# Performance work log

Measured on AMD Instinct MI355X. Metric: run time of the kernel, lower is better.

## Reference

```python
import jax, jax.numpy as jnp
import numpy as np

DIM = 512
HEADS = 8
HEAD_DIM = DIM // HEADS
WINDOW = 128
TOKEN_SELF_ATTN_VALUE = -5e4  # lucidrains local-attention constant for shared_qk self mask


def setup_inputs() -> dict:
    key = jax.random.key(0)
    k1, k2, k3, k4 = jax.random.split(key, 4)
    B, N = 4, 8192
    x = jax.random.normal(k1, (B, N, DIM), dtype=jnp.float32)
    w_qkv = jax.random.normal(k2, (3 * DIM, DIM), dtype=jnp.float32) * (DIM ** -0.5)
    w_proj = jax.random.normal(k3, (DIM, DIM), dtype=jnp.float32) * (DIM ** -0.5)
    b_proj = jax.random.normal(k4, (DIM,), dtype=jnp.float32) * 0.01
    return {"x": x, "w_qkv": w_qkv, "w_proj": w_proj, "b_proj": b_proj}


def _look_around(b):
    # b: [B,H,nw,w,D] -> [B,H,nw,2w,D] = concat(prev_window, cur_window); window 0 padded with zeros
    padded = jnp.pad(b, ((0, 0), (0, 0), (1, 0), (0, 0), (0, 0)))
    return jnp.concatenate([padded[:, :, :-1], b], axis=3)


def _local_attn(q, k, v):
    # causal sliding-window attention, window=128, look_backward=1, shared_qk
    B, H, N, D = q.shape
    w = WINDOW
    nw = N // w
    scale = D ** -0.5
    # shared_qk: l2-normalize keys (F.normalize, eps=1e-12)
    k = k / jnp.clip(jnp.linalg.norm(k, axis=-1, keepdims=True), 1e-12, None)

    bq = q.reshape(B, H, nw, w, D)
    bk = _look_around(k.reshape(B, H, nw, w, D))  # [B,H,nw,2w,D]
    bv = _look_around(v.reshape(B, H, nw, w, D))

    t = jnp.arange(N).reshape(nw, w)
    t_pad = jnp.pad(t, ((1, 0), (0, 0)), constant_values=-1)
    bq_t = t                                         # [nw, w]
    bq_k = jnp.concatenate([t_pad[:-1], t], axis=1)  # [nw, 2w]

    sim = jnp.einsum('bhwie,bhwje->bhwij', bq, bk) * scale  # [B,H,nw,w,2w]

    self_mask = bq_t[:, :, None] == bq_k[:, None, :]
    causal_mask = bq_t[:, :, None] < bq_k[:, None, :]
    pad_mask = (bq_k == -1)[:, None, :]
    mask_value = -jnp.finfo(sim.dtype).max
    sim = jnp.where(self_mask, TOKEN_SELF_ATTN_VALUE, sim)
    sim = jnp.where(causal_mask | pad_mask, mask_value, sim)

    attn = jax.nn.softmax(sim, axis=-1)  # dropout is identity in eval mode
    out = jnp.einsum('bhwij,bhwje->bhwie', attn, bv)
    return out.reshape(B, H, N, D)


def reference(x, w_qkv, w_proj, b_proj):
    B, N, C = x.shape
    qkv = x @ w_qkv.T  # [B,N,3C]
    q, k, v = jnp.split(qkv, 3, axis=-1)
    to_heads = lambda t: t.reshape(B, N, HEADS, HEAD_DIM).transpose(0, 2, 1, 3)
    out = _local_attn(to_heads(q), to_heads(k), to_heads(v))  # [B,H,N,D]
    out = out.transpose(0, 2, 1, 3).reshape(B, N, C)
    return out @ w_proj.T + b_proj
```

## Files before the change

### kernel.cpp

```cpp
#include <hip/hip_runtime.h>
#include <stdint.h>

typedef uint16_t u16;
typedef __bf16 bf16x8 __attribute__((ext_vector_type(8)));
typedef float f32x4 __attribute__((ext_vector_type(4)));
typedef uint16_t u16x4 __attribute__((ext_vector_type(4)));
typedef uint16_t u16x8 __attribute__((ext_vector_type(8)));

typedef __attribute__((address_space(1))) void as1_void;
typedef __attribute__((address_space(3))) void as3_void;

__device__ __forceinline__ float bf2f(u16 b) {
    union { uint32_t u; float f; } v; v.u = ((uint32_t)b) << 16; return v.f;
}
__device__ __forceinline__ u16 f2bf(float f) {
    union { float f; uint32_t u; } v; v.f = f;
    uint32_t u = v.u;
    u += 0x7fffu + ((u >> 16) & 1u);
    return (u16)(u >> 16);
}
__device__ __forceinline__ void gload_lds16(const u16* g, u16* l) {
    __builtin_amdgcn_global_load_lds((as1_void*)g, (as3_void*)l, 16, 0, 0);
}

__global__ __launch_bounds__(256) void cvt3(
    const float* __restrict__ x,  u16* __restrict__ xb,
    const float* __restrict__ wq, u16* __restrict__ wqb,
    const float* __restrict__ wp, u16* __restrict__ wpb)
{
    const float* src; u16* dst; int base, nb;
    const int b = blockIdx.x;
    if (b < 1024)      { src = x;  dst = xb;  base = b;        nb = 1024; }
    else if (b < 1072) { src = wq; dst = wqb; base = b - 1024; nb = 48;   }
    else               { src = wp; dst = wpb; base = b - 1072; nb = 16;   }
    size_t i = ((size_t)base * 256 + threadIdx.x) * 8;
    const size_t stride = (size_t)nb * 256 * 8;
    #pragma unroll
    for (int it = 0; it < 8; ++it, i += stride) {
        f32x4 a = *(const f32x4*)(src + i);
        f32x4 c = *(const f32x4*)(src + i + 4);
        u16x8 o;
        o[0] = f2bf(a[0]); o[1] = f2bf(a[1]); o[2] = f2bf(a[2]); o[3] = f2bf(a[3]);
        o[4] = f2bf(c[0]); o[5] = f2bf(c[1]); o[6] = f2bf(c[2]); o[7] = f2bf(c[3]);
        *(u16x8*)(dst + i) = o;
    }
}

template<int NT, bool C_F32, bool NORMK>
__global__ __launch_bounds__(256, 2) void gemm128(
    const u16* __restrict__ A, int lda,
    const u16* __restrict__ B, int ldb,
    const float* __restrict__ bias,
    void* __restrict__ Cv, int ldc)
{
    __shared__ u16 lA[2][128 * 64];
    __shared__ u16 lB[2][128 * 64];

    const int tid  = threadIdx.x;
    const int lane = tid & 63;
    const int wave = tid >> 6;
    const int wr = (wave >> 1) * 64;
    const int wc = (wave & 1) * 64;
    const int cl = lane & 15;
    const int gr = lane >> 4;

    int fid = blockIdx.y * gridDim.x + blockIdx.x;
    const int nwg = gridDim.x * gridDim.y;
    fid = (fid & 7) * (nwg >> 3) + (fid >> 3);
    const int row0 = (fid / gridDim.x) * 128;
    const int col0 = (fid % gridDim.x) * 128;

    const int srow   = lane >> 3;
    const int schunk = ((lane & 7) - srow) & 7;

    f32x4 acc[4][4] = {};

    auto STAGE = [&](int t, int d) {
        const int k0 = t * 64;
        #pragma unroll
        for (int i = 0; i < 4; ++i) {
            const int Rg = wave * 32 + i * 8;
            gload_lds16(A + (size_t)(row0 + Rg + srow) * lda + k0 + schunk * 8,
                        &lA[d][Rg * 64]);
            gload_lds16(B + (size_t)(col0 + Rg + srow) * ldb + k0 + schunk * 8,
                        &lB[d][Rg * 64]);
        }
    };

    auto COMPUTE = [&](int d) {
        const u16* la = lA[d];
        const u16* lb = lB[d];
        bf16x8 bfrag[2][4];
        #pragma unroll
        for (int kk = 0; kk < 2; ++kk)
            #pragma unroll
            for (int n = 0; n < 4; ++n) {
                const int rb = wc + n * 16 + cl;
                bfrag[kk][n] = *(const bf16x8*)(lb + rb * 64 + (((kk * 4 + gr + rb) & 7) * 8));
            }
        __builtin_amdgcn_s_setprio(1);
        #pragma unroll
        for (int m = 0; m < 4; ++m) {
            const int ra = wr + m * 16 + cl;
            const bf16x8 a0 = *(const bf16x8*)(la + ra * 64 + (((gr + ra) & 7) * 8));
            const bf16x8 a1 = *(const bf16x8*)(la + ra * 64 + (((4 + gr + ra) & 7) * 8));
            #pragma unroll
            for (int n = 0; n < 4; ++n)
                acc[m][n] = __builtin_amdgcn_mfma_f32_16x16x32_bf16(a0, bfrag[0][n], acc[m][n], 0, 0, 0);
            #pragma unroll
            for (int n = 0; n < 4; ++n)
                acc[m][n] = __builtin_amdgcn_mfma_f32_16x16x32_bf16(a1, bfrag[1][n], acc[m][n], 0, 0, 0);
        }
        __builtin_amdgcn_s_setprio(0);
    };

    STAGE(0, 0);
    STAGE(1, 1);
    #pragma unroll
    for (int t = 0; t < NT; ++t) {
        if (t < NT - 1) asm volatile("s_waitcnt vmcnt(8)" ::: "memory");
        else            asm volatile("s_waitcnt vmcnt(0)" ::: "memory");
        __builtin_amdgcn_s_barrier();
        COMPUTE(t & 1);
        __builtin_amdgcn_s_barrier();
        if (t + 2 < NT) STAGE(t + 2, t & 1);
    }

    if constexpr (NORMK) {
        if (col0 + wc >= 512 && col0 + wc < 1024) {
            #pragma unroll
            for (int m = 0; m < 4; ++m)
                #pragma unroll
                for (int j = 0; j < 4; ++j) {
                    float ss = 0.f;
                    #pragma unroll
                    for (int n = 0; n < 4; ++n) ss += acc[m][n][j] * acc[m][n][j];
                    ss += __shfl_xor(ss, 1);
                    ss += __shfl_xor(ss, 2);
                    ss += __shfl_xor(ss, 4);
                    ss += __shfl_xor(ss, 8);
                    const float scl = 1.f / fmaxf(sqrtf(ss), 1e-12f);
                    #pragma unroll
                    for (int n = 0; n < 4; ++n) acc[m][n][j] *= scl;
                }
        }
    }

    #pragma unroll
    for (int m = 0; m < 4; ++m) {
        const int r = row0 + wr + m * 16 + gr * 4;
        #pragma unroll
        for (int n = 0; n < 4; ++n) {
            const int c = col0 + wc + n * 16 + cl;
            const float bv = bias ? bias[c] : 0.f;
            #pragma unroll
            for (int j = 0; j < 4; ++j) {
                const float val = acc[m][n][j] + bv;
                if constexpr (C_F32) ((float*)Cv)[(size_t)(r + j) * ldc + c] = val;
                else                 ((u16*)Cv)[(size_t)(r + j) * ldc + c] = f2bf(val);
            }
        }
    }
}

template<bool A_F32, bool C_F32, bool NORMK>
__global__ __launch_bounds__(256) void gemm_bt_f32(
    const void* __restrict__ Av, int lda,
    const float* __restrict__ B, int ldb,
    const float* __restrict__ bias,
    void* __restrict__ Cv, int ldc,
    int K)
{
    __shared__ u16 lA[128 * 32];
    __shared__ u16 lB[128 * 32];

    const int tid  = threadIdx.x;
    const int lane = tid & 63;
    const int wave = tid >> 6;
    const int wr   = (wave >> 1) * 64;
    const int wc   = (wave & 1) * 64;
    const int row0 = blockIdx.y * 128;
    const int col0 = blockIdx.x * 128;

    f32x4 acc[4][4] = {};

    for (int k0 = 0; k0 < K; k0 += 32) {
        #pragma unroll
        for (int i = 0; i < 4; ++i) {
            const int idx = i * 256 + tid;
            const int r = idx >> 3;
            const int p = (idx & 7) * 4;
            u16x4 a4, b4;
            if constexpr (A_F32) {
                const float* Af = (const float*)Av;
                f32x4 va = *(const f32x4*)(Af + (size_t)(row0 + r) * lda + k0 + p);
                a4[0] = f2bf(va[0]); a4[1] = f2bf(va[1]); a4[2] = f2bf(va[2]); a4[3] = f2bf(va[3]);
            } else {
                const u16* Ab = (const u16*)Av;
                a4 = *(const u16x4*)(Ab + (size_t)(row0 + r) * lda + k0 + p);
            }
            {
                f32x4 vb = *(const f32x4*)(B + (size_t)(col0 + r) * ldb + k0 + p);
                b4[0] = f2bf(vb[0]); b4[1] = f2bf(vb[1]); b4[2] = f2bf(vb[2]); b4[3] = f2bf(vb[3]);
            }
            *(u16x4*)&lA[r * 32 + p] = a4;
            *(u16x4*)&lB[r * 32 + p] = b4;
        }
        __syncthreads();

        bf16x8 af[4], bfv[4];
        #pragma unroll
        for (int m = 0; m < 4; ++m)
            af[m] = *(const bf16x8*)(lA + (wr + m * 16 + (lane & 15)) * 32 + (lane >> 4) * 8);
        #pragma unroll
        for (int n = 0; n < 4; ++n)
            bfv[n] = *(const bf16x8*)(lB + (wc + n * 16 + (lane & 15)) * 32 + (lane >> 4) * 8);
        #pragma unroll
        for (int m = 0; m < 4; ++m)
            #pragma unroll
            for (int n = 0; n < 4; ++n)
                acc[m][n] = __builtin_amdgcn_mfma_f32_16x16x32_bf16(af[m], bfv[n], acc[m][n], 0, 0, 0);
        __syncthreads();
    }

    if constexpr (NORMK) {
        if (col0 >= 512 && col0 < 1024) {
            #pragma unroll
            for (int m = 0; m < 4; ++m)
                #pragma unroll
                for (int j = 0; j < 4; ++j) {
                    float ss = 0.f;
                    #pragma unroll
                    for (int n = 0; n < 4; ++n) ss += acc[m][n][j] * acc[m][n][j];
                    ss += __shfl_xor(ss, 1);
                    ss += __shfl_xor(ss, 2);
                    ss += __shfl_xor(ss, 4);
                    ss += __shfl_xor(ss, 8);
                    const float scl = 1.f / fmaxf(sqrtf(ss), 1e-12f);
                    #pragma unroll
                    for (int n = 0; n < 4; ++n) acc[m][n][j] *= scl;
                }
        }
    }

    #pragma unroll
    for (int m = 0; m < 4; ++m) {
        const int r = row0 + wr + m * 16 + ((lane >> 4) << 2);
        #pragma unroll
        for (int n = 0; n < 4; ++n) {
            const int c = col0 + wc + n * 16 + (lane & 15);
            const float bv = bias ? bias[c] : 0.f;
            #pragma unroll
            for (int j = 0; j < 4; ++j) {
                const float val = acc[m][n][j] + bv;
                if constexpr (C_F32) ((float*)Cv)[(size_t)(r + j) * ldc + c] = val;
                else                 ((u16*)Cv)[(size_t)(r + j) * ldc + c] = f2bf(val);
            }
        }
    }
}

__global__ __launch_bounds__(512, 4) void attn_kernel(const u16* qkv, u16* o)
{
    constexpr int CC = 1536;
    constexpr int NTOK = 8192;
    constexpr int KP = 72;
    constexpr int VP = 136;
    constexpr int PP = 136;
    __shared__ u16 kn[128 * KP];
    __shared__ u16 vT[64 * VP];
    __shared__ u16 Pl[128 * PP];

    const int tid  = threadIdx.x;
    const int lane = tid & 63;
    const int wave = tid >> 6;
    const int cl = lane & 15;
    const int gr = lane >> 4;

    int blk = blockIdx.x;
    blk = (blk & 7) * (gridDim.x >> 3) + (blk >> 3);

    const int iw  = blk & 63;
    const int h   = (blk >> 6) & 7;
    const int b   = blk >> 9;

    const int tq0 = iw * 128;
    const size_t rowbase = (size_t)b * NTOK;
    const u16* qbase = qkv + rowbase * CC + h * 64;
    const u16* kbase = qbase + 512;
    const u16* vbase = qbase + 1024;

    const int wrow = wave * 16;
    bf16x8 qf[2];
    #pragma unroll
    for (int kk = 0; kk < 2; ++kk)
        qf[kk] = *(const bf16x8*)(qbase + (size_t)(tq0 + wrow + cl) * CC + kk * 32 + gr * 8);

    f32x4 oacc[4] = {};
    float m_run[4] = {-3.0e38f, -3.0e38f, -3.0e38f, -3.0e38f};
    float l_run[4] = {0.f, 0.f, 0.f, 0.f};

    for (int c = 0; c < 2; ++c) {
        const int tkc = tq0 - 128 + c * 128;

        #pragma unroll
        for (int p = 0; p < 2; ++p) {
            const int id = tid + p * 512;
            const int row = id >> 3, dc = id & 7;
            u16x8 v8 = {};
            if (tkc >= 0) v8 = *(const u16x8*)(kbase + (size_t)(tkc + row) * CC + dc * 8);
            *(u16x8*)&kn[row * KP + dc * 8] = v8;
        }
        #pragma unroll
        for (int p = 0; p < 2; ++p) {
            const int id = tid + p * 512;
            const int key = id & 127, dc = id >> 7;
            u16x8 v8 = {};
            if (tkc >= 0) v8 = *(const u16x8*)(vbase + (size_t)(tkc + key) * CC + dc * 8);
            #pragma unroll
            for (int e = 0; e < 8; ++e) vT[(dc * 8 + e) * VP + key] = v8[e];
        }
        __syncthreads();

        f32x4 s[8] = {};
        #pragma unroll
        for (int n = 0; n < 8; ++n)
            #pragma unroll
            for (int kk = 0; kk < 2; ++kk) {
                const bf16x8 kf = *(const bf16x8*)&kn[(n * 16 + cl) * KP + kk * 32 + gr * 8];
                s[n] = __builtin_amdgcn_mfma_f32_16x16x32_bf16(qf[kk], kf, s[n], 0, 0, 0);
            }

        float pmax[4] = {-3.0e38f, -3.0e38f, -3.0e38f, -3.0e38f};
        #pragma unroll
        for (int n = 0; n < 8; ++n) {
            const int tkk = tkc + n * 16 + cl;
            const bool pad = tkk < 0;
            #pragma unroll
            for (int j = 0; j < 4; ++j) {
                const int tq = tq0 + wrow + gr * 4 + j;
                float sv = s[n][j] * 0.125f;
                const int rel = tkk - tq;
                sv = (rel == 0) ? -5.0e4f : sv;
                sv = (rel > 0 || pad) ? -6.0e4f : sv;
                s[n][j] = sv;
                pmax[j] = fmaxf(pmax[j], sv);
            }
        }
        float cold[4];
        #pragma unroll
        for (int j = 0; j < 4; ++j) {
            pmax[j] = fmaxf(pmax[j], __shfl_xor(pmax[j], 1));
            pmax[j] = fmaxf(pmax[j], __shfl_xor(pmax[j], 2));
            pmax[j] = fmaxf(pmax[j], __shfl_xor(pmax[j], 4));
            pmax[j] = fmaxf(pmax[j], __shfl_xor(pmax[j], 8));
            const float mn = fmaxf(m_run[j], pmax[j]);
            cold[j] = __expf(m_run[j] - mn);
            m_run[j] = mn;
            l_run[j] *= cold[j];
        }
        #pragma unroll
        for (int n = 0; n < 8; ++n)
            #pragma unroll
            for (int j = 0; j < 4; ++j) {
                const float p = __expf(s[n][j] - m_run[j]);
                s[n][j] = p;
                l_run[j] += p;
            }
        #pragma unroll
        for (int n = 0; n < 4; ++n) {
            f32x4 t = oacc[n];
            t[0] *= cold[0]; t[1] *= cold[1]; t[2] *= cold[2]; t[3] *= cold[3];
            oacc[n] = t;
        }
        #pragma unroll
        for (int n = 0; n < 8; ++n)
            #pragma unroll
            for (int j = 0; j < 4; ++j)
                Pl[(wrow + gr * 4 + j) * PP + n * 16 + cl] = f2bf(s[n][j]);
        __syncthreads();

        #pragma unroll
        for (int kk = 0; kk < 4; ++kk) {
            const bf16x8 pa = *(const bf16x8*)&Pl[(wrow + cl) * PP + kk * 32 + gr * 8];
            #pragma unroll
            for (int n = 0; n < 4; ++n) {
                const bf16x8 vb = *(const bf16x8*)&vT[(n * 16 + cl) * VP + kk * 32 + gr * 8];
                oacc[n] = __builtin_amdgcn_mfma_f32_16x16x32_bf16(pa, vb, oacc[n], 0, 0, 0);
            }
        }
        __syncthreads();
    }

    float inv[4];
    #pragma unroll
    for (int j = 0; j < 4; ++j) {
        l_run[j] += __shfl_xor(l_run[j], 1);
        l_run[j] += __shfl_xor(l_run[j], 2);
        l_run[j] += __shfl_xor(l_run[j], 4);
        l_run[j] += __shfl_xor(l_run[j], 8);
        inv[j] = 1.f / l_run[j];
    }
    u16* obase = o + rowbase * CC + h * 64;
    const int r0 = tq0 + wrow + gr * 4;
    #pragma unroll
    for (int n = 0; n < 4; ++n) {
        const int d = n * 16 + cl;
        #pragma unroll
        for (int j = 0; j < 4; ++j)
            obase[(size_t)(r0 + j) * CC + d] = f2bf(oacc[n][j] * inv[j]);
    }
}

extern "C" void kernel_launch(void* const* d_in, const int* in_sizes, int n_in,
                              void* d_out, int out_size, void* d_ws, size_t ws_size,
                              hipStream_t stream)
{
    (void)in_sizes; (void)n_in; (void)out_size;
    const float* x      = (const float*)d_in[0];
    const float* w_qkv  = (const float*)d_in[1];
    const float* w_proj = (const float*)d_in[2];
    const float* b_proj = (const float*)d_in[3];
    float* out = (float*)d_out;

    const int BN = 4 * 8192;
    const size_t qkv_b = (size_t)BN * 1536 * 2;
    const size_t xb_b  = (size_t)BN * 512 * 2;
    const size_t wq_b  = (size_t)1536 * 512 * 2;
    const size_t wp_b  = (size_t)512 * 512 * 2;

    uint8_t* p = (uint8_t*)d_ws;
    u16* qkv = (u16*)p;

    if (ws_size >= qkv_b + xb_b + wq_b + wp_b) {
        u16* xb  = (u16*)(p + qkv_b);
        u16* wqb = (u16*)(p + qkv_b + xb_b);
        u16* wpb = (u16*)(p + qkv_b + xb_b + wq_b);
        cvt3<<<1088, 256, 0, stream>>>(x, xb, w_qkv, wqb, w_proj, wpb);
        gemm128<8, false, true><<<dim3(12, 256), 256, 0, stream>>>(
            xb, 512, wqb, 512, nullptr, qkv, 1536);
        attn_kernel<<<dim3(4 * 8 * 64), 512, 0, stream>>>(qkv, qkv);
        gemm128<8, true, false><<<dim3(4, 256), 256, 0, stream>>>(
            qkv, 1536, wpb, 512, b_proj, out, 512);
    } else {
        gemm_bt_f32<true, false, true><<<dim3(12, BN / 128), 256, 0, stream>>>(
            x, 512, w_qkv, 512, nullptr, qkv, 1536, 512);
        attn_kernel<<<dim3(4 * 8 * 64), 512, 0, stream>>>(qkv, qkv);
        gemm_bt_f32<false, true, false><<<dim3(4, BN / 128), 256, 0, stream>>>(
            qkv, 1536, w_proj, 512, b_proj, out, 512, 512);
    }
}
```

Before: 190.0 us.

## Load GEMM B operand directly into registers instead of staging through LDS

The bf16 GEMM no longer stages the weight (B) tile in shared memory. Each wave now loads its B fragments straight from global memory into registers, software-prefetched one k-step ahead, while A is still double-buffered in LDS. This halves LDS usage and the LDS read traffic per block and removes the B cooperative loads. The cost is redundant global/L2 reads of B across the waves and blocks that share it, more registers held live, and hand-tuned vmcnt wait counts that must match the new number of outstanding loads.

```diff
diff --git a/kernel.cpp b/kernel.cpp
--- a/kernel.cpp
+++ b/kernel.cpp
@@ -47,14 +47,13 @@
 }
 
 template<int NT, bool C_F32, bool NORMK>
-__global__ __launch_bounds__(256, 2) void gemm128(
+__global__ __launch_bounds__(256, 2) void gemm_breg(
     const u16* __restrict__ A, int lda,
     const u16* __restrict__ B, int ldb,
     const float* __restrict__ bias,
     void* __restrict__ Cv, int ldc)
 {
     __shared__ u16 lA[2][128 * 64];
-    __shared__ u16 lB[2][128 * 64];
 
     const int tid  = threadIdx.x;
     const int lane = tid & 63;
@@ -73,6 +72,8 @@
     const int srow   = lane >> 3;
     const int schunk = ((lane & 7) - srow) & 7;
 
+    const u16* Bb = B + (size_t)(col0 + wc + cl) * ldb + gr * 8;
+
     f32x4 acc[4][4] = {};
 
     auto STAGE = [&](int t, int d) {
@@ -82,46 +83,49 @@
             const int Rg = wave * 32 + i * 8;
             gload_lds16(A + (size_t)(row0 + Rg + srow) * lda + k0 + schunk * 8,
                         &lA[d][Rg * 64]);
-            gload_lds16(B + (size_t)(col0 + Rg + srow) * ldb + k0 + schunk * 8,
-                        &lB[d][Rg * 64]);
-        }
-    };
-
-    auto COMPUTE = [&](int d) {
-        const u16* la = lA[d];
-        const u16* lb = lB[d];
-        bf16x8 bfrag[2][4];
-        #pragma unroll
-        for (int kk = 0; kk < 2; ++kk)
-            #pragma unroll
-            for (int n = 0; n < 4; ++n) {
-                const int rb = wc + n * 16 + cl;
-                bfrag[kk][n] = *(const bf16x8*)(lb + rb * 64 + (((kk * 4 + gr + rb) & 7) * 8));
-            }
-        __builtin_amdgcn_s_setprio(1);
-        #pragma unroll
-        for (int m = 0; m < 4; ++m) {
-            const int ra = wr + m * 16 + cl;
-            const bf16x8 a0 = *(const bf16x8*)(la + ra * 64 + (((gr + ra) & 7) * 8));
-            const bf16x8 a1 = *(const bf16x8*)(la + ra * 64 + (((4 + gr + ra) & 7) * 8));
-            #pragma unroll
-            for (int n = 0; n < 4; ++n)
-                acc[m][n] = __builtin_amdgcn_mfma_f32_16x16x32_bf16(a0, bfrag[0][n], acc[m][n], 0, 0, 0);
-            #pragma unroll
-            for (int n = 0; n < 4; ++n)
-                acc[m][n] = __builtin_amdgcn_mfma_f32_16x16x32_bf16(a1, bfrag[1][n], acc[m][n], 0, 0, 0);
-        }
-        __builtin_amdgcn_s_setprio(0);
+        }
     };
 
     STAGE(0, 0);
     STAGE(1, 1);
+    bf16x8 bq[4], bqn[4];
+    #pragma unroll
+    for (int n = 0; n < 4; ++n) bq[n] = *(const bf16x8*)(Bb + (size_t)(n * 16) * ldb);
+
     #pragma unroll
     for (int t = 0; t < NT; ++t) {
-        if (t < NT - 1) asm volatile("s_waitcnt vmcnt(8)" ::: "memory");
-        else            asm volatile("s_waitcnt vmcnt(0)" ::: "memory");
+        if (t == 0)           asm volatile("s_waitcnt vmcnt(8)"  ::: "memory");
+        else if (t == 1)      asm volatile("s_waitcnt vmcnt(16)" ::: "memory");
+        else if (t < NT - 1)  asm volatile("s_waitcnt vmcnt(12)" ::: "memory");
+        else                  asm volatile("s_waitcnt vmcnt(8)"  ::: "memory");
         __builtin_amdgcn_s_barrier();
-        COMPUTE(t & 1);
+        const u16* la = lA[t & 1];
+
+        #pragma unroll
+        for (int kk = 0; kk < 2; ++kk) {
+            bf16x8 af[4];
+            #pragma unroll
+            for (int m = 0; m < 4; ++m) {
+                const int ra = wr + m * 16 + cl;
+                af[m] = *(const bf16x8*)(la + ra * 64 + (((kk * 4 + gr + ra) & 7) * 8));
+            }
+            {
+                int knext = t * 64 + kk * 32 + 32;
+                if (knext >= NT * 64) knext = 0;
+                #pragma unroll
+                for (int n = 0; n < 4; ++n)
+                    bqn[n] = *(const bf16x8*)(Bb + (size_t)(n * 16) * ldb + knext);
+            }
+            __builtin_amdgcn_s_setprio(1);
+            #pragma unroll
+            for (int m = 0; m < 4; ++m)
+                #pragma unroll
+                for (int n = 0; n < 4; ++n)
+                    acc[m][n] = __builtin_amdgcn_mfma_f32_16x16x32_bf16(af[m], bq[n], acc[m][n], 0, 0, 0);
+            __builtin_amdgcn_s_setprio(0);
+            #pragma unroll
+            for (int n = 0; n < 4; ++n) bq[n] = bqn[n];
+        }
         __builtin_amdgcn_s_barrier();
         if (t + 2 < NT) STAGE(t + 2, t & 1);
     }
@@ -437,10 +441,10 @@
         u16* wqb = (u16*)(p + qkv_b + xb_b);
         u16* wpb = (u16*)(p + qkv_b + xb_b + wq_b);
         cvt3<<<1088, 256, 0, stream>>>(x, xb, w_qkv, wqb, w_proj, wpb);
-        gemm128<8, false, true><<<dim3(12, 256), 256, 0, stream>>>(
+        gemm_breg<8, false, true><<<dim3(12, 256), 256, 0, stream>>>(
             xb, 512, wqb, 512, nullptr, qkv, 1536);
         attn_kernel<<<dim3(4 * 8 * 64), 512, 0, stream>>>(qkv, qkv);
-        gemm128<8, true, false><<<dim3(4, 256), 256, 0, stream>>>(
+        gemm_breg<8, true, false><<<dim3(4, 256), 256, 0, stream>>>(
             qkv, 1536, wpb, 512, b_proj, out, 512);
     } else {
         gemm_bt_f32<true, false, true><<<dim3(12, BN / 128), 256, 0, stream>>>(
```

Result: slower. 243.4 us (+28.1%).

## Deepen GEMM pipeline to four K32 stages and prefetch attention K/V chunk

Applied to the files above, without the earlier changes.

The bf16 GEMM now uses four LDS buffers of K=32 slices with three tiles in flight instead of two K=64 buffers. LDS fragment reads for the next step are issued before the barrier, so each iteration needs one barrier instead of two. The attention kernel loads the second key/value chunk into registers while the first chunk is being computed, hiding global latency. In exchange there are twice as many loop iterations with fewer MFMAs each, and the register prefetch raises VGPR pressure.

```diff
diff --git a/kernel.cpp b/kernel.cpp
--- a/kernel.cpp
+++ b/kernel.cpp
@@ -47,14 +47,14 @@
 }
 
 template<int NT, bool C_F32, bool NORMK>
-__global__ __launch_bounds__(256, 2) void gemm128(
+__global__ __launch_bounds__(256, 2) void gemm_pipe(
     const u16* __restrict__ A, int lda,
     const u16* __restrict__ B, int ldb,
     const float* __restrict__ bias,
     void* __restrict__ Cv, int ldc)
 {
-    __shared__ u16 lA[2][128 * 64];
-    __shared__ u16 lB[2][128 * 64];
+    __shared__ u16 lA[4][128 * 32];
+    __shared__ u16 lB[4][128 * 32];
 
     const int tid  = threadIdx.x;
     const int lane = tid & 63;
@@ -70,60 +70,58 @@
     const int row0 = (fid / gridDim.x) * 128;
     const int col0 = (fid % gridDim.x) * 128;
 
-    const int srow   = lane >> 3;
-    const int schunk = ((lane & 7) - srow) & 7;
-
     f32x4 acc[4][4] = {};
 
     auto STAGE = [&](int t, int d) {
-        const int k0 = t * 64;
-        #pragma unroll
-        for (int i = 0; i < 4; ++i) {
-            const int Rg = wave * 32 + i * 8;
-            gload_lds16(A + (size_t)(row0 + Rg + srow) * lda + k0 + schunk * 8,
-                        &lA[d][Rg * 64]);
-            gload_lds16(B + (size_t)(col0 + Rg + srow) * ldb + k0 + schunk * 8,
-                        &lB[d][Rg * 64]);
+        const int k0 = t * 32;
+        #pragma unroll
+        for (int i = 0; i < 2; ++i) {
+            const int id  = i * 256 + tid;
+            const int row = id >> 2;
+            const int sch = ((id & 3) - ((row >> 1) & 3)) & 3;
+            gload_lds16(A + (size_t)(row0 + row) * lda + k0 + sch * 8, &lA[d][id * 8]);
+            gload_lds16(B + (size_t)(col0 + row) * ldb + k0 + sch * 8, &lB[d][id * 8]);
         }
     };
 
-    auto COMPUTE = [&](int d) {
-        const u16* la = lA[d];
-        const u16* lb = lB[d];
-        bf16x8 bfrag[2][4];
-        #pragma unroll
-        for (int kk = 0; kk < 2; ++kk)
-            #pragma unroll
-            for (int n = 0; n < 4; ++n) {
-                const int rb = wc + n * 16 + cl;
-                bfrag[kk][n] = *(const bf16x8*)(lb + rb * 64 + (((kk * 4 + gr + rb) & 7) * 8));
-            }
-        __builtin_amdgcn_s_setprio(1);
+    bf16x8 af[4], bfv[4];
+    auto READS = [&](int t) {
+        const u16* la = lA[t & 3];
+        const u16* lb = lB[t & 3];
         #pragma unroll
         for (int m = 0; m < 4; ++m) {
             const int ra = wr + m * 16 + cl;
-            const bf16x8 a0 = *(const bf16x8*)(la + ra * 64 + (((gr + ra) & 7) * 8));
-            const bf16x8 a1 = *(const bf16x8*)(la + ra * 64 + (((4 + gr + ra) & 7) * 8));
+            af[m] = *(const bf16x8*)&la[ra * 32 + ((gr + (ra >> 1)) & 3) * 8];
+        }
+        #pragma unroll
+        for (int n = 0; n < 4; ++n) {
+            const int rb = wc + n * 16 + cl;
+            bfv[n] = *(const bf16x8*)&lb[rb * 32 + ((gr + (rb >> 1)) & 3) * 8];
+        }
+    };
+
+    STAGE(0, 0); STAGE(1, 1); STAGE(2, 2);
+    asm volatile("s_waitcnt vmcnt(4)" ::: "memory");
+    __builtin_amdgcn_s_barrier();
+    READS(0);
+
+    #pragma unroll
+    for (int t = 0; t < NT; ++t) {
+        if (t + 3 < NT) STAGE(t + 3, (t + 3) & 3);
+        __builtin_amdgcn_s_setprio(1);
+        #pragma unroll
+        for (int m = 0; m < 4; ++m)
             #pragma unroll
             for (int n = 0; n < 4; ++n)
-                acc[m][n] = __builtin_amdgcn_mfma_f32_16x16x32_bf16(a0, bfrag[0][n], acc[m][n], 0, 0, 0);
-            #pragma unroll
-            for (int n = 0; n < 4; ++n)
-                acc[m][n] = __builtin_amdgcn_mfma_f32_16x16x32_bf16(a1, bfrag[1][n], acc[m][n], 0, 0, 0);
-        }
+                acc[m][n] = __builtin_amdgcn_mfma_f32_16x16x32_bf16(af[m], bfv[n], acc[m][n], 0, 0, 0);
         __builtin_amdgcn_s_setprio(0);
-    };
-
-    STAGE(0, 0);
-    STAGE(1, 1);
-    #pragma unroll
-    for (int t = 0; t < NT; ++t) {
-        if (t < NT - 1) asm volatile("s_waitcnt vmcnt(8)" ::: "memory");
-        else            asm volatile("s_waitcnt vmcnt(0)" ::: "memory");
-        __builtin_amdgcn_s_barrier();
-        COMPUTE(t & 1);
-        __builtin_amdgcn_s_barrier();
-        if (t + 2 < NT) STAGE(t + 2, t & 1);
+        if (t + 1 < NT) READS(t + 1);
+        if (t < NT - 1) {
+            asm volatile("s_waitcnt lgkmcnt(0)" ::: "memory");
+            if (t + 3 < NT) asm volatile("s_waitcnt vmcnt(4)" ::: "memory");
+            else            asm volatile("s_waitcnt vmcnt(0)" ::: "memory");
+            __builtin_amdgcn_s_barrier();
+        }
     }
 
     if constexpr (NORMK) {
@@ -285,6 +283,8 @@
     const int b   = blk >> 9;
 
     const int tq0 = iw * 128;
+    const int tkc0 = tq0 - 128;
+    const int tkc1 = tq0;
     const size_t rowbase = (size_t)b * NTOK;
     const u16* qbase = qkv + rowbase * CC + h * 64;
     const u16* kbase = qbase + 512;
@@ -300,28 +300,7 @@
     float m_run[4] = {-3.0e38f, -3.0e38f, -3.0e38f, -3.0e38f};
     float l_run[4] = {0.f, 0.f, 0.f, 0.f};
 
-    for (int c = 0; c < 2; ++c) {
-        const int tkc = tq0 - 128 + c * 128;
-
-        #pragma unroll
-        for (int p = 0; p < 2; ++p) {
-            const int id = tid + p * 512;
-            const int row = id >> 3, dc = id & 7;
-            u16x8 v8 = {};
-            if (tkc >= 0) v8 = *(const u16x8*)(kbase + (size_t)(tkc + row) * CC + dc * 8);
-            *(u16x8*)&kn[row * KP + dc * 8] = v8;
-        }
-        #pragma unroll
-        for (int p = 0; p < 2; ++p) {
-            const int id = tid + p * 512;
-            const int key = id & 127, dc = id >> 7;
-            u16x8 v8 = {};
-            if (tkc >= 0) v8 = *(const u16x8*)(vbase + (size_t)(tkc + key) * CC + dc * 8);
-            #pragma unroll
-            for (int e = 0; e < 8; ++e) vT[(dc * 8 + e) * VP + key] = v8[e];
-        }
-        __syncthreads();
-
+    auto CHUNK = [&](int tkc) {
         f32x4 s[8] = {};
         #pragma unroll
         for (int n = 0; n < 8; ++n)
@@ -330,7 +309,6 @@
                 const bf16x8 kf = *(const bf16x8*)&kn[(n * 16 + cl) * KP + kk * 32 + gr * 8];
                 s[n] = __builtin_amdgcn_mfma_f32_16x16x32_bf16(qf[kk], kf, s[n], 0, 0, 0);
             }
-
         float pmax[4] = {-3.0e38f, -3.0e38f, -3.0e38f, -3.0e38f};
         #pragma unroll
         for (int n = 0; n < 8; ++n) {
@@ -379,7 +357,6 @@
             for (int j = 0; j < 4; ++j)
                 Pl[(wrow + gr * 4 + j) * PP + n * 16 + cl] = f2bf(s[n][j]);
         __syncthreads();
-
         #pragma unroll
         for (int kk = 0; kk < 4; ++kk) {
             const bf16x8 pa = *(const bf16x8*)&Pl[(wrow + cl) * PP + kk * 32 + gr * 8];
@@ -389,8 +366,52 @@
                 oacc[n] = __builtin_amdgcn_mfma_f32_16x16x32_bf16(pa, vb, oacc[n], 0, 0, 0);
             }
         }
-        __syncthreads();
-    }
+    };
+
+    #pragma unroll
+    for (int p = 0; p < 2; ++p) {
+        const int id = tid + p * 512;
+        const int row = id >> 3, dc = id & 7;
+        u16x8 v8 = {};
+        if (tkc0 >= 0) v8 = *(const u16x8*)(kbase + (size_t)(tkc0 + row) * CC + dc * 8);
+        *(u16x8*)&kn[row * KP + dc * 8] = v8;
+    }
+    #pragma unroll
+    for (int p = 0; p < 2; ++p) {
+        const int id = tid + p * 512;
+        const int key = id & 127, dc = id >> 7;
+        u16x8 v8 = {};
+        if (tkc0 >= 0) v8 = *(const u16x8*)(vbase + (size_t)(tkc0 + key) * CC + dc * 8);
+        #pragma unroll
+        for (int e = 0; e < 8; ++e) vT[(dc * 8 + e) * VP + key] = v8[e];
+    }
+    u16x8 kr[2], vr[2];
+    #pragma unroll
+    for (int p = 0; p < 2; ++p) {
+        const int id = tid + p * 512;
+        kr[p] = *(const u16x8*)(kbase + (size_t)(tkc1 + (id >> 3)) * CC + (id & 7) * 8);
+        vr[p] = *(const u16x8*)(vbase + (size_t)(tkc1 + (id & 127)) * CC + (id >> 7) * 8);
+    }
+    __syncthreads();
+
+    CHUNK(tkc0);
+    __syncthreads();
+
+    #pragma unroll
+    for (int p = 0; p < 2; ++p) {
+        const int id = tid + p * 512;
+        *(u16x8*)&kn[(id >> 3) * KP + (id & 7) * 8] = kr[p];
+    }
+    #pragma unroll
+    for (int p = 0; p < 2; ++p) {
+        const int id = tid + p * 512;
+        const int key = id & 127, dc = id >> 7;
+        #pragma unroll
+        for (int e = 0; e < 8; ++e) vT[(dc * 8 + e) * VP + key] = vr[p][e];
+    }
+    __syncthreads();
+
+    CHUNK(tkc1);
 
     float inv[4];
     #pragma unroll
@@ -437,10 +458,10 @@
         u16* wqb = (u16*)(p + qkv_b + xb_b);
         u16* wpb = (u16*)(p + qkv_b + xb_b + wq_b);
         cvt3<<<1088, 256, 0, stream>>>(x, xb, w_qkv, wqb, w_proj, wpb);
-        gemm128<8, false, true><<<dim3(12, 256), 256, 0, stream>>>(
+        gemm_pipe<16, false, true><<<dim3(12, 256), 256, 0, stream>>>(
             xb, 512, wqb, 512, nullptr, qkv, 1536);
         attn_kernel<<<dim3(4 * 8 * 64), 512, 0, stream>>>(qkv, qkv);
-        gemm128<8, true, false><<<dim3(4, 256), 256, 0, stream>>>(
+        gemm_pipe<16, true, false><<<dim3(4, 256), 256, 0, stream>>>(
             qkv, 1536, wpb, 512, b_proj, out, 512);
     } else {
         gemm_bt_f32<true, false, true><<<dim3(12, BN / 128), 256, 0, stream>>>(
```

Result: faster. 181.5 us (-4.5%).
